# Optimization experiments

Hardware: AMD Instinct MI355X
Metric: run time of the kernel (lower is better)

## Reference

```python
import jax, jax.numpy as jnp
import numpy as np
from jax import lax

B, H, W, C, NH = 16, 64, 64, 192, 6


def rope2d(x, h, w, c, base=10000.0):
    # 2D RoPE: channel_dims=(h,w), k_max = c // 4; angles (h,w,c//2)
    kmax = c // 4
    theta = 1.0 / (base ** (jnp.arange(kmax, dtype=jnp.float32) / kmax))
    ai = jnp.broadcast_to(jnp.arange(h, dtype=jnp.float32)[:, None, None] * theta, (h, w, kmax))
    aj = jnp.broadcast_to(jnp.arange(w, dtype=jnp.float32)[None, :, None] * theta, (h, w, kmax))
    ang = jnp.concatenate([ai, aj], axis=-1)  # (h,w,c//2)
    cos, sin = jnp.cos(ang), jnp.sin(ang)
    xr = x.reshape(*x.shape[:-1], c // 2, 2)
    xe, xo = xr[..., 0], xr[..., 1]
    # complex multiply (cos + i sin) * (xe + i xo)
    return jnp.stack([xe * cos - xo * sin, xe * sin + xo * cos], axis=-1).reshape(x.shape)


def setup_inputs() -> dict:
    key = jax.random.key(0)
    ks = jax.random.split(key, 4)
    return {
        "x": jax.random.normal(ks[0], (B, H, W, C), dtype=jnp.float32),
        "qk_w": jax.random.normal(ks[1], (2 * C, C), dtype=jnp.float32) * 0.02,
        "qk_b": jnp.zeros((2 * C,), dtype=jnp.float32),
        "lepe_w": jax.random.normal(ks[2], (C, 1, 3, 3), dtype=jnp.float32) * 0.1,
        "lepe_b": jnp.zeros((C,), dtype=jnp.float32),
    }


def reference(x, qk_w, qk_b, lepe_w, lepe_b):
    b, h, w, c = x.shape
    n = h * w
    nh = NH
    d = c // nh
    qk = x @ qk_w.T + qk_b  # (b,h,w,2c)
    q = jax.nn.elu(qk[..., :c]) + 1.0
    k = jax.nn.elu(qk[..., c:]) + 1.0
    q_rope = rope2d(q, h, w, c).reshape(b, n, nh, d).transpose(0, 2, 1, 3)  # (b,nh,n,d)
    k_rope = rope2d(k, h, w, c).reshape(b, n, nh, d).transpose(0, 2, 1, 3)
    qh = q.reshape(b, n, nh, d).transpose(0, 2, 1, 3)
    kh = k.reshape(b, n, nh, d).transpose(0, 2, 1, 3)
    vh = x.reshape(b, n, nh, d).transpose(0, 2, 1, 3)  # v = x
    kmean = kh.mean(axis=2)  # (b,nh,d)
    z = 1.0 / (jnp.einsum('bhnd,bhd->bhn', qh, kmean)[..., None] + 1e-6)  # (b,nh,n,1)
    scale = 1.0 / jnp.sqrt(jnp.float32(n))
    kv = jnp.einsum('bhnd,bhne->bhde', k_rope * scale, vh * scale)  # (b,nh,d,d)
    out = jnp.einsum('bhnd,bhde->bhne', q_rope, kv) * z  # (b,nh,n,d)
    out = out.transpose(0, 2, 1, 3).reshape(b, n, c)
    # LePE: depthwise 3x3 conv on v (= x) in NCHW
    v_nchw = x.transpose(0, 3, 1, 2)
    lepe = lax.conv_general_dilated(v_nchw, lepe_w, (1, 1), 'SAME',
                                    dimension_numbers=('NCHW', 'OIHW', 'NCHW'),
                                    feature_group_count=c)
    lepe = lepe + lepe_b[None, :, None, None]
    return out + lepe.transpose(0, 2, 3, 1).reshape(b, n, c)
```

## Files before the change

kernel.cpp:

```cpp
#include <hip/hip_runtime.h>
#include <hip/hip_bf16.h>

using short8   = __attribute__((ext_vector_type(8))) short;
using floatx4  = __attribute__((ext_vector_type(4))) float;
using floatx16 = __attribute__((ext_vector_type(16))) float;

#define CC 192
#define CN 4096
#define NHEAD 6
#define DHEAD 32
#define NZERO (16 * NHEAD * DHEAD * DHEAD + 16 * NHEAD * DHEAD)
#define ZBLK ((NZERO + 255) / 256)
#define TBLK ((CN * 96 + 255) / 256)

__device__ __forceinline__ float bf2f(short s) {
    return __uint_as_float(((unsigned)(unsigned short)s) << 16);
}
__device__ __forceinline__ short f2bf(float f) {
    __hip_bfloat16 h = __float2bfloat16(f);
    return *(short*)&h;
}

__global__ void k0_all(float* __restrict__ zp, unsigned* __restrict__ tabp,
                       const float* __restrict__ qkw, __hip_bfloat16* __restrict__ wfr)
{
    int bid = blockIdx.x;
    if (bid < ZBLK) {
        int i = bid * 256 + threadIdx.x;
        if (i < NZERO) zp[i] = 0.f;
    } else if (bid < ZBLK + TBLK) {
        int idx = (bid - ZBLK) * 256 + threadIdx.x;
        if (idx >= CN * 96) return;
        int n = idx / 96, c2 = idx - n * 96;
        int h = n >> 6, w = n & 63;
        int i = (c2 < 48) ? c2 : c2 - 48;
        float pos = (float)((c2 < 48) ? h : w);
        float theta = expf(-(float)i * (9.210340371976184f / 48.0f));
        float ang = pos * theta;
        unsigned c = (unsigned)(unsigned short)f2bf(cosf(ang));
        unsigned s = (unsigned)(unsigned short)f2bf(sinf(ang));
        tabp[idx] = c | (s << 16);
    } else {
        int tid = (bid - ZBLK - TBLK) * 256 + threadIdx.x;
        if (tid >= 24 * 6 * 64) return;
        int lane = tid & 63;
        int ks = (tid >> 6) % 6;
        int nig = tid / (6 * 64);
        int col = nig * 16 + (lane & 15);
        int k = ks * 32 + (lane >> 4) * 8;
        const float4* src = (const float4*)(qkw + (long)col * CC + k);
        float4 f0 = src[0], f1 = src[1];
        short8 s;
        s[0] = f2bf(f0.x); s[1] = f2bf(f0.y); s[2] = f2bf(f0.z); s[3] = f2bf(f0.w);
        s[4] = f2bf(f1.x); s[5] = f2bf(f1.y); s[6] = f2bf(f1.z); s[7] = f2bf(f1.w);
        *(short8*)&wfr[(long)tid * 8] = s;
    }
}

__global__ __launch_bounds__(512)
void k1_gemm(const float* __restrict__ x, const __hip_bfloat16* __restrict__ wfr,
             const float* __restrict__ qkb,
             __hip_bfloat16* __restrict__ qws, __hip_bfloat16* __restrict__ kws,
             __hip_bfloat16* __restrict__ xbf)
{
    __shared__ __align__(16) short A_lds[128 * 200];
    __shared__ __align__(16) short B_lds[24 * 512];

    const int tid  = threadIdx.x;
    const int wid  = tid >> 6, lane = tid & 63;
    const int wm   = wid >> 1, wn = wid & 1;
    const int lrow = lane & 15;
    const int l4   = lane >> 4;
    const long rowBase = (long)blockIdx.x * 128;

#pragma unroll
    for (int it = 0; it < 6; ++it) {
        int slot = it * 512 + tid;
        int row = slot / 24, c0 = (slot - (slot / 24) * 24) * 8;
        const float4* src = (const float4*)(x + (rowBase + row) * CC + c0);
        float4 f0 = src[0], f1 = src[1];
        short8 s;
        s[0] = f2bf(f0.x); s[1] = f2bf(f0.y); s[2] = f2bf(f0.z); s[3] = f2bf(f0.w);
        s[4] = f2bf(f1.x); s[5] = f2bf(f1.y); s[6] = f2bf(f1.z); s[7] = f2bf(f1.w);
        *(short8*)&A_lds[row * 200 + c0] = s;
        *(short8*)&xbf[(rowBase + row) * CC + c0] = s;
    }

    floatx4 acc[2][12];
#pragma unroll
    for (int i = 0; i < 2; ++i)
#pragma unroll
        for (int j = 0; j < 12; ++j) acc[i][j] = (floatx4)0.f;

    for (int ks = 0; ks < 6; ++ks) {
        short8 bst[3];
#pragma unroll
        for (int j = 0; j < 3; ++j) {
            int s = j * 512 + tid;
            bst[j] = *(const short8*)&wfr[((long)((s >> 6) * 6 + ks) * 64 + (s & 63)) * 8];
        }
        __syncthreads();
#pragma unroll
        for (int j = 0; j < 3; ++j) {
            int s = j * 512 + tid;
            *(short8*)&B_lds[s * 8] = bst[j];
        }
        __syncthreads();

        short8 a0 = *(const short8*)&A_lds[(wm * 32 + lrow) * 200 + ks * 32 + l4 * 8];
        short8 a1 = *(const short8*)&A_lds[(wm * 32 + 16 + lrow) * 200 + ks * 32 + l4 * 8];
#pragma unroll
        for (int ni = 0; ni < 12; ++ni) {
            short8 bf = *(const short8*)&B_lds[(wn * 12 + ni) * 512 + lane * 8];
            acc[0][ni] = __builtin_amdgcn_mfma_f32_16x16x32_bf16(a0, bf, acc[0][ni], 0, 0, 0);
            acc[1][ni] = __builtin_amdgcn_mfma_f32_16x16x32_bf16(a1, bf, acc[1][ni], 0, 0, 0);
        }
    }

    __hip_bfloat16* dstbase = wn ? kws : qws;
#pragma unroll
    for (int ni = 0; ni < 12; ++ni) {
        int col_l = ni * 16 + lrow;
        float bias = qkb[wn * 192 + col_l];
#pragma unroll
        for (int mi = 0; mi < 2; ++mi) {
#pragma unroll
            for (int r = 0; r < 4; ++r) {
                int rowl = wm * 32 + mi * 16 + l4 * 4 + r;
                long rowg = rowBase + rowl;
                float v = acc[mi][ni][r] + bias;
                v = (v > 0.f) ? (v + 1.f) : expf(v);
                dstbase[rowg * CC + col_l] = __float2bfloat16(v);
            }
        }
    }
}

__global__ __launch_bounds__(256)
void k2_kv(const __hip_bfloat16* __restrict__ kws, const __hip_bfloat16* __restrict__ xbf,
           const unsigned* __restrict__ tabp, float* __restrict__ kv, float* __restrict__ kmean)
{
    int bid = blockIdx.x;
    int chunk = bid & 7;
    int hd = (bid >> 3) % NHEAD;
    int b = bid / (8 * NHEAD);
    int tid = threadIdx.x;
    int lane = tid & 63, wave = tid >> 6;

    __shared__ __align__(16) short S[8192];
    __shared__ float km_s[32];
    char* krT = (char*)S;
    char* vT  = (char*)S + 8192;

    if (tid < 32) km_s[tid] = 0.f;

    const int krow = tid >> 2, kq = tid & 3;

    floatx16 acc = (floatx16)0.f;
    float msum[8];
#pragma unroll
    for (int j = 0; j < 8; ++j) msum[j] = 0.f;

    const int n0 = chunk * 512;
    const long rb = (long)b * CN;

    short8 k8[2], v8[2];
    uint4  u[2];
#pragma unroll
    for (int p = 0; p < 2; ++p) {
        int n = n0 + p * 64 + krow;
        k8[p] = *(const short8*)&kws[(rb + n) * CC + hd * DHEAD + kq * 8];
        v8[p] = *(const short8*)&xbf[(rb + n) * CC + hd * DHEAD + kq * 8];
        u[p]  = *(const uint4*)&tabp[(long)n * 96 + hd * 16 + kq * 4];
    }

    for (int batch = 0; batch < 4; ++batch) {
        if (batch) __syncthreads();
#pragma unroll
        for (int p = 0; p < 2; ++p) {
            int r = p * 64 + krow;
            float kf[8];
#pragma unroll
            for (int j = 0; j < 8; ++j) { kf[j] = bf2f(k8[p][j]); msum[j] += kf[j]; }
            float cs[4], sn[4];
            cs[0] = bf2f((short)(u[p].x & 0xffff)); sn[0] = bf2f((short)(u[p].x >> 16));
            cs[1] = bf2f((short)(u[p].y & 0xffff)); sn[1] = bf2f((short)(u[p].y >> 16));
            cs[2] = bf2f((short)(u[p].z & 0xffff)); sn[2] = bf2f((short)(u[p].z >> 16));
            cs[3] = bf2f((short)(u[p].w & 0xffff)); sn[3] = bf2f((short)(u[p].w >> 16));
            short kr8[8];
#pragma unroll
            for (int q = 0; q < 4; ++q) {
                kr8[2*q]   = f2bf(kf[2*q] * cs[q] - kf[2*q+1] * sn[q]);
                kr8[2*q+1] = f2bf(kf[2*q] * sn[q] + kf[2*q+1] * cs[q]);
            }
#pragma unroll
            for (int j = 0; j < 8; ++j) {
                int ch = kq * 8 + j;
                int byte = (ch * 256 + r * 2) ^ (j << 4);
                *(short*)(krT + byte) = kr8[j];
                *(short*)(vT  + byte) = v8[p][j];
            }
        }
        if (batch < 3) {
#pragma unroll
            for (int p = 0; p < 2; ++p) {
                int n = n0 + (batch + 1) * 128 + p * 64 + krow;
                k8[p] = *(const short8*)&kws[(rb + n) * CC + hd * DHEAD + kq * 8];
                v8[p] = *(const short8*)&xbf[(rb + n) * CC + hd * DHEAD + kq * 8];
                u[p]  = *(const uint4*)&tabp[(long)n * 96 + hd * 16 + kq * 4];
            }
        }
        __syncthreads();
        const int d = lane & 31;
        const int kh = (lane >> 5) * 8;
#pragma unroll
        for (int s = 0; s < 2; ++s) {
            int k = wave * 32 + s * 16 + kh;
            int abyte = (d * 256 + k * 2) ^ ((d & 7) << 4);
            short8 af = *(const short8*)(krT + abyte);
            short8 bf = *(const short8*)(vT + abyte);
            acc = __builtin_amdgcn_mfma_f32_32x32x16_bf16(af, bf, acc, 0, 0, 0);
        }
    }
    __syncthreads();

    float* red = (float*)S;
#pragma unroll
    for (int r = 0; r < 16; ++r)
        red[(wave * 16 + r) * 64 + lane] = acc[r];
#pragma unroll
    for (int j = 0; j < 8; ++j) {
        float m = msum[j];
        m += __shfl_down(m, 32);
        m += __shfl_down(m, 16);
        m += __shfl_down(m, 8);
        m += __shfl_down(m, 4);
        if (lane < 4) atomicAdd(&km_s[(tid & 3) * 8 + j], m);
    }
    __syncthreads();

    const float sc = 1.f / 4096.f;
    {
        float* kvb = kv + (long)(b * NHEAD + hd) * DHEAD * DHEAD;
        const int l = tid & 63;
        const int rbase = (tid >> 6) * 4;
#pragma unroll
        for (int i = 0; i < 4; ++i) {
            int r = rbase + i;
            float v = red[(0 * 16 + r) * 64 + l] + red[(1 * 16 + r) * 64 + l]
                    + red[(2 * 16 + r) * 64 + l] + red[(3 * 16 + r) * 64 + l];
            int row = (r & 3) + 8 * (r >> 2) + 4 * (l >> 5);
            int col = l & 31;
            atomicAdd(&kvb[row * DHEAD + col], v * sc);
        }
    }
    if (tid < 32) atomicAdd(&kmean[(b * NHEAD + hd) * DHEAD + tid], km_s[tid] * sc);
}

__global__ __launch_bounds__(256)
void k3_out(const __hip_bfloat16* __restrict__ qws, const __hip_bfloat16* __restrict__ xbf,
            const unsigned* __restrict__ tabp, const float* __restrict__ kv,
            const float* __restrict__ kmean, const float* __restrict__ lw,
            const float* __restrict__ lb, float* __restrict__ out)
{
    int raw = blockIdx.x;
    int bid = (raw & 7) * 128 + (raw >> 3);
    int b = bid >> 6, h = bid & 63;
    int tid = threadIdx.x;
    int wave = tid >> 6, lane = tid & 63, lrow = lane & 15, l4 = lane >> 4;

    __shared__ __align__(16) __hip_bfloat16 qa[64][104];
    __shared__ __align__(16) __hip_bfloat16 kvt[NHEAD][32][36];
    __shared__ __align__(16) float lwT[9][192];
    __shared__ float lb_lds[CC];
    __shared__ float km_lds[CC];
    __shared__ float zden[64][8];

    const long nbase = (long)b * CN + h * 64;

    const float* kvsrc = kv + (long)b * NHEAD * DHEAD * DHEAD;
    for (int i = tid; i < NHEAD * DHEAD * DHEAD; i += 256) {
        int hd = i >> 10, d = (i >> 5) & 31, e = i & 31;
        kvt[hd][e][d] = __float2bfloat16(kvsrc[i]);
    }
    if (tid < CC) { km_lds[tid] = kmean[b * CC + tid]; lb_lds[tid] = lb[tid]; }
    for (int i = tid; i < CC * 9; i += 256) {
        int c = i / 9, tap = i - c * 9;
        lwT[tap][c] = lw[i];
    }
    __syncthreads();

#pragma unroll
    for (int half = 0; half < 2; ++half) {
#pragma unroll
        for (int it = 0; it < 3; ++it) {
            int slot = it * 256 + tid;
            int w = slot / 12;
            int sub = slot - w * 12;
            int c0 = half * 96 + sub * 8;
            short8 qv = *(const short8*)&qws[(nbase + w) * CC + c0];
            float q[8];
#pragma unroll
            for (int j = 0; j < 8; ++j) q[j] = bf2f(qv[j]);
            float p = 0.f;
#pragma unroll
            for (int j = 0; j < 8; ++j) p += q[j] * km_lds[c0 + j];
            p += __shfl_xor(p, 1);
            p += __shfl_xor(p, 2);
            if ((sub & 3) == 0) zden[w][half * 3 + (sub >> 2)] = p;
            int n = h * 64 + w;
            uint4 u = *(const uint4*)&tabp[(long)n * 96 + (c0 >> 1)];
            float4 t0, t1;
            t0.x = bf2f((short)(u.x & 0xffff)); t0.y = bf2f((short)(u.x >> 16));
            t0.z = bf2f((short)(u.y & 0xffff)); t0.w = bf2f((short)(u.y >> 16));
            t1.x = bf2f((short)(u.z & 0xffff)); t1.y = bf2f((short)(u.z >> 16));
            t1.z = bf2f((short)(u.w & 0xffff)); t1.w = bf2f((short)(u.w >> 16));
            short8 qr;
            qr[0] = f2bf(q[0]*t0.x - q[1]*t0.y);  qr[1] = f2bf(q[0]*t0.y + q[1]*t0.x);
            qr[2] = f2bf(q[2]*t0.z - q[3]*t0.w);  qr[3] = f2bf(q[2]*t0.w + q[3]*t0.z);
            qr[4] = f2bf(q[4]*t1.x - q[5]*t1.y);  qr[5] = f2bf(q[4]*t1.y + q[5]*t1.x);
            qr[6] = f2bf(q[6]*t1.z - q[7]*t1.w);  qr[7] = f2bf(q[6]*t1.w + q[7]*t1.z);
            *(short8*)&qa[w][sub * 8] = qr;
        }
        __syncthreads();

        const int rt = wave;
        const int wbase = rt * 16 + l4 * 4;
#pragma unroll
        for (int hl = 0; hl < 3; ++hl) {
            int hd = half * 3 + hl;
            short8 a = *(const short8*)&qa[rt * 16 + lrow][hl * 32 + l4 * 8];
            float zv[4];
#pragma unroll
            for (int r = 0; r < 4; ++r) zv[r] = 1.f / (zden[wbase + r][hd] + 1e-6f);
#pragma unroll
            for (int nt = 0; nt < 2; ++nt) {
                short8 bfr = *(const short8*)&kvt[hd][nt * 16 + lrow][l4 * 8];
                floatx4 acc = __builtin_amdgcn_mfma_f32_16x16x32_bf16(a, bfr, (floatx4)0.f, 0, 0, 0);
                int col_l = hl * 32 + nt * 16 + lrow;
#pragma unroll
                for (int r = 0; r < 4; ++r)
                    qa[wbase + r][col_l] = __float2bfloat16(acc[r] * zv[r]);
            }
        }
        __syncthreads();

#pragma unroll
        for (int it = 0; it < 3; ++it) {
            int slot = it * 256 + tid;
            int w = slot / 12;
            int g = slot - w * 12;
            int c0g = g * 8;
            int c0 = half * 96 + c0g;
            float vals[8];
#pragma unroll
            for (int j = 0; j < 8; ++j) vals[j] = lb_lds[c0 + j];
#pragma unroll
            for (int dy = 0; dy < 3; ++dy) {
                int hy = h + dy - 1;
                if (hy < 0 || hy > 63) continue;
                const short* base = (const short*)xbf + (((long)b * 64 + hy) * 64) * CC + c0;
#pragma unroll
                for (int dx = 0; dx < 3; ++dx) {
                    int wx = w + dx - 1;
                    if (wx < 0 || wx > 63) continue;
                    short8 xv = *(const short8*)&base[(long)wx * CC];
                    const float4* wt4 = (const float4*)&lwT[dy * 3 + dx][c0];
                    float4 wa = wt4[0], wb = wt4[1];
                    vals[0] += bf2f(xv[0]) * wa.x;  vals[1] += bf2f(xv[1]) * wa.y;
                    vals[2] += bf2f(xv[2]) * wa.z;  vals[3] += bf2f(xv[3]) * wa.w;
                    vals[4] += bf2f(xv[4]) * wb.x;  vals[5] += bf2f(xv[5]) * wb.y;
                    vals[6] += bf2f(xv[6]) * wb.z;  vals[7] += bf2f(xv[7]) * wb.w;
                }
            }
            short8 at = *(const short8*)&qa[w][c0g];
#pragma unroll
            for (int j = 0; j < 8; ++j) vals[j] += bf2f(at[j]);
            float4 o0, o1;
            o0.x = vals[0]; o0.y = vals[1]; o0.z = vals[2]; o0.w = vals[3];
            o1.x = vals[4]; o1.y = vals[5]; o1.z = vals[6]; o1.w = vals[7];
            float* op = &out[(nbase + w) * CC + c0];
            *(float4*)op = o0;
            *(float4*)(op + 4) = o1;
        }
        __syncthreads();
    }
}

extern "C" void kernel_launch(void* const* d_in, const int* in_sizes, int n_in,
                              void* d_out, int out_size, void* d_ws, size_t ws_size,
                              hipStream_t stream)
{
    const float* x   = (const float*)d_in[0];
    const float* qkw = (const float*)d_in[1];
    const float* qkb = (const float*)d_in[2];
    const float* lw  = (const float*)d_in[3];
    const float* lb  = (const float*)d_in[4];
    float* out = (float*)d_out;

    char* ws = (char*)d_ws;
    unsigned* tabp = (unsigned*)ws;            ws += (size_t)CN * 96 * 4;
    __hip_bfloat16* qws = (__hip_bfloat16*)ws; ws += (size_t)16 * CN * CC * 2;
    __hip_bfloat16* kws = (__hip_bfloat16*)ws; ws += (size_t)16 * CN * CC * 2;
    __hip_bfloat16* xbf = (__hip_bfloat16*)ws; ws += (size_t)16 * CN * CC * 2;
    __hip_bfloat16* wfr = (__hip_bfloat16*)ws; ws += (size_t)24 * 6 * 64 * 8 * 2;
    float* kv = (float*)ws;                    ws += (size_t)16 * NHEAD * DHEAD * DHEAD * 4;
    float* km = (float*)ws;                    ws += (size_t)16 * NHEAD * DHEAD * 4;

    const int wblk = (24 * 6 * 64 + 255) / 256;
    k0_all<<<ZBLK + TBLK + wblk, 256, 0, stream>>>(kv, tabp, qkw, wfr);
    k1_gemm<<<512, 512, 0, stream>>>(x, wfr, qkb, qws, kws, xbf);
    k2_kv<<<16 * NHEAD * 8, 256, 0, stream>>>(kws, xbf, tabp, kv, km);
    k3_out<<<16 * 64, 256, 0, stream>>>(qws, xbf, tabp, kv, km, lw, lb, out);
}
```

Measured before the change: 91.49 us.

## Shrink RoPE table to separable 1D table and re-swizzle K/V LDS stores

Replaces the full per-position cos/sin table (4096x96 entries) with a separable 64x48 table indexed by row or column position, since the 2D RoPE angle depends only on h for the first half of channels and on w for the second. This cuts table generation work in the setup kernel and the table traffic read by the kv and output kernels. It also changes the LDS XOR swizzle in the kv kernel to mix in the quad index, meant to reduce bank conflicts on the transposed scalar stores. The table loads now depend on head index and position, which adds a branch.

```diff
diff --git a/kernel.cpp b/kernel.cpp
--- a/kernel.cpp
+++ b/kernel.cpp
@@ -11,7 +11,7 @@
 #define DHEAD 32
 #define NZERO (16 * NHEAD * DHEAD * DHEAD + 16 * NHEAD * DHEAD)
 #define ZBLK ((NZERO + 255) / 256)
-#define TBLK ((CN * 96 + 255) / 256)
+#define TABN 12
 
 __device__ __forceinline__ float bf2f(short s) {
     return __uint_as_float(((unsigned)(unsigned short)s) << 16);
@@ -21,27 +21,24 @@
     return *(short*)&h;
 }
 
-__global__ void k0_all(float* __restrict__ zp, unsigned* __restrict__ tabp,
+__global__ void k0_all(float* __restrict__ zp, unsigned* __restrict__ tabs,
                        const float* __restrict__ qkw, __hip_bfloat16* __restrict__ wfr)
 {
     int bid = blockIdx.x;
     if (bid < ZBLK) {
         int i = bid * 256 + threadIdx.x;
         if (i < NZERO) zp[i] = 0.f;
-    } else if (bid < ZBLK + TBLK) {
+    } else if (bid < ZBLK + TABN) {
         int idx = (bid - ZBLK) * 256 + threadIdx.x;
-        if (idx >= CN * 96) return;
-        int n = idx / 96, c2 = idx - n * 96;
-        int h = n >> 6, w = n & 63;
-        int i = (c2 < 48) ? c2 : c2 - 48;
-        float pos = (float)((c2 < 48) ? h : w);
+        if (idx >= 64 * 48) return;
+        int pos = idx / 48, i = idx - pos * 48;
         float theta = expf(-(float)i * (9.210340371976184f / 48.0f));
-        float ang = pos * theta;
+        float ang = (float)pos * theta;
         unsigned c = (unsigned)(unsigned short)f2bf(cosf(ang));
         unsigned s = (unsigned)(unsigned short)f2bf(sinf(ang));
-        tabp[idx] = c | (s << 16);
+        tabs[idx] = c | (s << 16);
     } else {
-        int tid = (bid - ZBLK - TBLK) * 256 + threadIdx.x;
+        int tid = (bid - ZBLK - TABN) * 256 + threadIdx.x;
         if (tid >= 24 * 6 * 64) return;
         int lane = tid & 63;
         int ks = (tid >> 6) % 6;
@@ -138,7 +135,7 @@
 
 __global__ __launch_bounds__(256)
 void k2_kv(const __hip_bfloat16* __restrict__ kws, const __hip_bfloat16* __restrict__ xbf,
-           const unsigned* __restrict__ tabp, float* __restrict__ kv, float* __restrict__ kmean)
+           const unsigned* __restrict__ tabs, float* __restrict__ kv, float* __restrict__ kmean)
 {
     int bid = blockIdx.x;
     int chunk = bid & 7;
@@ -165,13 +162,11 @@
     const long rb = (long)b * CN;
 
     short8 k8[2], v8[2];
-    uint4  u[2];
 #pragma unroll
     for (int p = 0; p < 2; ++p) {
         int n = n0 + p * 64 + krow;
         k8[p] = *(const short8*)&kws[(rb + n) * CC + hd * DHEAD + kq * 8];
         v8[p] = *(const short8*)&xbf[(rb + n) * CC + hd * DHEAD + kq * 8];
-        u[p]  = *(const uint4*)&tabp[(long)n * 96 + hd * 16 + kq * 4];
     }
 
     for (int batch = 0; batch < 4; ++batch) {
@@ -179,14 +174,19 @@
 #pragma unroll
         for (int p = 0; p < 2; ++p) {
             int r = p * 64 + krow;
+            int nbase = n0 + batch * 128 + p * 64;
+            int hpos = nbase >> 6;
+            uint4 u = (hd < 3)
+                ? *(const uint4*)&tabs[hpos * 48 + hd * 16 + kq * 4]
+                : *(const uint4*)&tabs[krow * 48 + (hd - 3) * 16 + kq * 4];
             float kf[8];
 #pragma unroll
             for (int j = 0; j < 8; ++j) { kf[j] = bf2f(k8[p][j]); msum[j] += kf[j]; }
             float cs[4], sn[4];
-            cs[0] = bf2f((short)(u[p].x & 0xffff)); sn[0] = bf2f((short)(u[p].x >> 16));
-            cs[1] = bf2f((short)(u[p].y & 0xffff)); sn[1] = bf2f((short)(u[p].y >> 16));
-            cs[2] = bf2f((short)(u[p].z & 0xffff)); sn[2] = bf2f((short)(u[p].z >> 16));
-            cs[3] = bf2f((short)(u[p].w & 0xffff)); sn[3] = bf2f((short)(u[p].w >> 16));
+            cs[0] = bf2f((short)(u.x & 0xffff)); sn[0] = bf2f((short)(u.x >> 16));
+            cs[1] = bf2f((short)(u.y & 0xffff)); sn[1] = bf2f((short)(u.y >> 16));
+            cs[2] = bf2f((short)(u.z & 0xffff)); sn[2] = bf2f((short)(u.z >> 16));
+            cs[3] = bf2f((short)(u.w & 0xffff)); sn[3] = bf2f((short)(u.w >> 16));
             short kr8[8];
 #pragma unroll
             for (int q = 0; q < 4; ++q) {
@@ -196,7 +196,8 @@
 #pragma unroll
             for (int j = 0; j < 8; ++j) {
                 int ch = kq * 8 + j;
-                int byte = (ch * 256 + r * 2) ^ (j << 4);
+                int g = j ^ (kq << 1);
+                int byte = (ch * 256 + r * 2) ^ (g << 4);
                 *(short*)(krT + byte) = kr8[j];
                 *(short*)(vT  + byte) = v8[p][j];
             }
@@ -207,16 +208,16 @@
                 int n = n0 + (batch + 1) * 128 + p * 64 + krow;
                 k8[p] = *(const short8*)&kws[(rb + n) * CC + hd * DHEAD + kq * 8];
                 v8[p] = *(const short8*)&xbf[(rb + n) * CC + hd * DHEAD + kq * 8];
-                u[p]  = *(const uint4*)&tabp[(long)n * 96 + hd * 16 + kq * 4];
             }
         }
         __syncthreads();
         const int d = lane & 31;
         const int kh = (lane >> 5) * 8;
+        const int gd = (d & 7) ^ (((d >> 3) & 3) << 1);
 #pragma unroll
         for (int s = 0; s < 2; ++s) {
             int k = wave * 32 + s * 16 + kh;
-            int abyte = (d * 256 + k * 2) ^ ((d & 7) << 4);
+            int abyte = (d * 256 + k * 2) ^ (gd << 4);
             short8 af = *(const short8*)(krT + abyte);
             short8 bf = *(const short8*)(vT + abyte);
             acc = __builtin_amdgcn_mfma_f32_32x32x16_bf16(af, bf, acc, 0, 0, 0);
@@ -259,7 +260,7 @@
 
 __global__ __launch_bounds__(256)
 void k3_out(const __hip_bfloat16* __restrict__ qws, const __hip_bfloat16* __restrict__ xbf,
-            const unsigned* __restrict__ tabp, const float* __restrict__ kv,
+            const unsigned* __restrict__ tabs, const float* __restrict__ kv,
             const float* __restrict__ kmean, const float* __restrict__ lw,
             const float* __restrict__ lb, float* __restrict__ out)
 {
@@ -308,8 +309,9 @@
             p += __shfl_xor(p, 1);
             p += __shfl_xor(p, 2);
             if ((sub & 3) == 0) zden[w][half * 3 + (sub >> 2)] = p;
-            int n = h * 64 + w;
-            uint4 u = *(const uint4*)&tabp[(long)n * 96 + (c0 >> 1)];
+            uint4 u = (half == 0)
+                ? *(const uint4*)&tabs[h * 48 + sub * 4]
+                : *(const uint4*)&tabs[w * 48 + sub * 4];
             float4 t0, t1;
             t0.x = bf2f((short)(u.x & 0xffff)); t0.y = bf2f((short)(u.x >> 16));
             t0.z = bf2f((short)(u.y & 0xffff)); t0.w = bf2f((short)(u.y >> 16));
@@ -399,7 +401,7 @@
     float* out = (float*)d_out;
 
     char* ws = (char*)d_ws;
-    unsigned* tabp = (unsigned*)ws;            ws += (size_t)CN * 96 * 4;
+    unsigned* tabs = (unsigned*)ws;            ws += (size_t)64 * 48 * 4;
     __hip_bfloat16* qws = (__hip_bfloat16*)ws; ws += (size_t)16 * CN * CC * 2;
     __hip_bfloat16* kws = (__hip_bfloat16*)ws; ws += (size_t)16 * CN * CC * 2;
     __hip_bfloat16* xbf = (__hip_bfloat16*)ws; ws += (size_t)16 * CN * CC * 2;
@@ -408,8 +410,8 @@
     float* km = (float*)ws;                    ws += (size_t)16 * NHEAD * DHEAD * 4;
 
     const int wblk = (24 * 6 * 64 + 255) / 256;
-    k0_all<<<ZBLK + TBLK + wblk, 256, 0, stream>>>(kv, tabp, qkw, wfr);
+    k0_all<<<ZBLK + TABN + wblk, 256, 0, stream>>>(kv, tabs, qkw, wfr);
     k1_gemm<<<512, 512, 0, stream>>>(x, wfr, qkb, qws, kws, xbf);
-    k2_kv<<<16 * NHEAD * 8, 256, 0, stream>>>(kws, xbf, tabp, kv, km);
-    k3_out<<<16 * 64, 256, 0, stream>>>(qws, xbf, tabp, kv, km, lw, lb, out);
-}
+    k2_kv<<<16 * NHEAD * 8, 256, 0, stream>>>(kws, xbf, tabs, kv, km);
+    k3_out<<<16 * 64, 256, 0, stream>>>(qws, xbf, tabs, kv, km, lw, lb, out);
+}
```

Result: faster. 89.13 us (-2.6%).
